# Performance work log

Measured on AMD Instinct MI355X. Metric: run time of the kernel, lower is better.

Reference implementation:

```python
import jax, jax.numpy as jnp
import numpy as np


def setup_inputs() -> dict:
    key = jax.random.key(0)
    k1, k2 = jax.random.split(key)
    x = jax.random.normal(k1, (32, 256, 32, 32), dtype=jnp.float32)
    emb = jax.random.uniform(k2, (256, 2048), dtype=jnp.float32)
    return {"x": x, "emb": emb}


def reference(x, emb):
    # x: (B, D, H, W), emb: (D, K)
    B, D = x.shape[0], x.shape[1]
    spatial = x.shape[2:]
    K = emb.shape[1]
    # flatten latents: (N, D) with N = B*H*W
    xf = jnp.moveaxis(x, 1, -1).reshape(-1, D)
    d2 = (jnp.sum(xf * xf, axis=-1, keepdims=True)
          - 2.0 * (xf @ emb)
          + jnp.sum(emb * emb, axis=0))  # (N, K)
    argmin = jnp.argmin(d2, axis=-1)  # (N,)
    q = jnp.take(emb.T, argmin, axis=0)  # (N, D) nearest codes
    out = q.reshape(B, *spatial, D)
    out = jnp.moveaxis(out, -1, 1)  # (B, D, H, W)
    return out
```

## Files before the change

### kernel.cpp

```cpp
#include <hip/hip_runtime.h>


typedef __attribute__((ext_vector_type(8))) _Float16 half8v;
typedef __attribute__((ext_vector_type(16))) float floatx16;
typedef unsigned int uint;
typedef unsigned short ushort;

#define DD 256
#define KK 2048
#define SS 1024
#define NN 32768
#define MT 64
#define NTT 256
#define LDA 24
#define MFMA_F16 __builtin_amdgcn_mfma_f32_32x32x16_f16

#define XSLAB  262144
#define XPLANE 131072
#define EPLANE 262144

union HU { _Float16 f; ushort u; };

__device__ __forceinline__ void split16(float v, ushort& h, ushort& l) {
    HU a, b;
    a.f = (_Float16)v;
    b.f = (_Float16)(v - (float)a.f);
    h = a.u; l = b.u;
}

__global__ __launch_bounds__(256) void hn_kernel(const float* __restrict__ emb,
                                                 float* __restrict__ hn) {
    int k = blockIdx.x * 256 + threadIdx.x;
    float a = 0.f;
#pragma unroll 32
    for (int d = 0; d < DD; ++d) { float e = emb[d * KK + k]; a += e * e; }
    hn[k] = 0.5f * a;
}

__global__ __launch_bounds__(256) void pack_emb(const float* __restrict__ emb,
                                                uint* __restrict__ epk) {
    int idx = blockIdx.x * 256 + threadIdx.x;
    int k = idx & (KK - 1);
    int d2 = idx >> 11;
    float a = emb[(size_t)(2 * d2) * KK + k];
    float b = emb[(size_t)(2 * d2 + 1) * KK + k];
    ushort h0, l0, h1, l1;
    split16(a, h0, l0);
    split16(b, h1, l1);
    epk[idx] = (uint)h0 | ((uint)h1 << 16);
    epk[EPLANE + idx] = (uint)l0 | ((uint)l1 << 16);
}

__global__ __launch_bounds__(256) void pack_x(const float* __restrict__ x,
                                              uint* __restrict__ px) {
    int idx = blockIdx.x * 256 + threadIdx.x;
    int s4 = idx & 255;
    int d2 = (idx >> 8) & 127;
    int bq = idx >> 15;
    const float4* xp = reinterpret_cast<const float4*>(
        x + ((size_t)(bq * DD + 2 * d2)) * SS) + s4;
    float4 a = xp[0];
    float4 b = xp[SS / 4];
    ushort h0, l0, h1, l1;
    uint4 th, tl;
    split16(a.x, h0, l0); split16(b.x, h1, l1);
    th.x = (uint)h0 | ((uint)h1 << 16); tl.x = (uint)l0 | ((uint)l1 << 16);
    split16(a.y, h0, l0); split16(b.y, h1, l1);
    th.y = (uint)h0 | ((uint)h1 << 16); tl.y = (uint)l0 | ((uint)l1 << 16);
    split16(a.z, h0, l0); split16(b.z, h1, l1);
    th.z = (uint)h0 | ((uint)h1 << 16); tl.z = (uint)l0 | ((uint)l1 << 16);
    split16(a.w, h0, l0); split16(b.w, h1, l1);
    th.w = (uint)h0 | ((uint)h1 << 16); tl.w = (uint)l0 | ((uint)l1 << 16);
    size_t o4 = (size_t)bq * (XSLAB / 4) + (size_t)d2 * (SS / 4) + s4;
    reinterpret_cast<uint4*>(px)[o4] = th;
    reinterpret_cast<uint4*>(px)[o4 + XPLANE / 4] = tl;
}

template <bool PRE>
__global__ __launch_bounds__(512, 4) void vq_fused(
        const float* __restrict__ x, const float* __restrict__ emb,
        const float* __restrict__ hn, const uint* __restrict__ epk,
        float* out) {
    __shared__ ushort Ah[2][MT * LDA], Al[2][MT * LDA];
    __shared__ ushort Bh[2][NTT * LDA], Bl[2][NTT * LDA];
    __shared__ float sv[4][MT];
    __shared__ int   sc[4][MT];
    __shared__ int   bc[MT];

    const int tid = threadIdx.x;
    const int lane = tid & 63;
    const int wid = tid >> 6;
    const int colk = lane & 31;
    const int half = lane >> 5;
    const int wm = (wid & 1) * 32;
    const int wn = (wid >> 1) * 64;

    const int base_n = blockIdx.x * MT;
    const int bq = base_n >> 10;
    const int sb = base_n & (SS - 1);

    const int lat_a = tid & 63;
    const int dqa2 = tid >> 6;
    const int cod_b = tid & 255;
    const int dqb = (tid >> 8) * 8;
    const int dqb2 = (tid >> 8) * 4;

    const float* xb = x + ((size_t)bq * DD + 2 * dqa2) * SS + sb + lat_a;
    const uint* aH = reinterpret_cast<const uint*>(out)
                     + (size_t)bq * XSLAB + (size_t)dqa2 * SS + sb + lat_a;
    const uint* eH = epk + (size_t)dqb2 * KK + cod_b;

    floatx16 acc[2];
#pragma unroll
    for (int j = 0; j < 2; ++j) acc[j] = (floatx16)(0.0f);

    float bestv[16];
    int bestc[16];
#pragma unroll
    for (int r = 0; r < 16; ++r) { bestv[r] = 3.4e38f; bestc[r] = 0; }

    float fa[2], fb[8];
    uint ua[2], ub[8];
    if constexpr (PRE) {
        ua[0] = aH[0];
        ua[1] = aH[XPLANE];
#pragma unroll
        for (int i = 0; i < 4; ++i) {
            ub[i] = eH[(size_t)i * KK];
            ub[4 + i] = eH[EPLANE + (size_t)i * KK];
        }
    } else {
        fa[0] = xb[0];
        fa[1] = xb[SS];
        const float* p = emb + (size_t)dqb * KK + cod_b;
#pragma unroll
        for (int i = 0; i < 8; ++i) fb[i] = p[(size_t)i * KK];
    }
    if constexpr (PRE) {
        *reinterpret_cast<uint*>(&Ah[0][lat_a * LDA + dqa2 * 2]) = ua[0];
        *reinterpret_cast<uint*>(&Al[0][lat_a * LDA + dqa2 * 2]) = ua[1];
        uint4 t;
        t.x = ub[0]; t.y = ub[1]; t.z = ub[2]; t.w = ub[3];
        *reinterpret_cast<uint4*>(&Bh[0][cod_b * LDA + dqb]) = t;
        t.x = ub[4]; t.y = ub[5]; t.z = ub[6]; t.w = ub[7];
        *reinterpret_cast<uint4*>(&Bl[0][cod_b * LDA + dqb]) = t;
    } else {
        ushort h[8], l[8];
        split16(fa[0], h[0], l[0]);
        split16(fa[1], h[1], l[1]);
        *reinterpret_cast<uint*>(&Ah[0][lat_a * LDA + dqa2 * 2]) =
            (uint)h[0] | ((uint)h[1] << 16);
        *reinterpret_cast<uint*>(&Al[0][lat_a * LDA + dqa2 * 2]) =
            (uint)l[0] | ((uint)l[1] << 16);
#pragma unroll
        for (int i = 0; i < 8; ++i) split16(fb[i], h[i], l[i]);
        uint4 t;
        t.x = (uint)h[0] | ((uint)h[1] << 16);
        t.y = (uint)h[2] | ((uint)h[3] << 16);
        t.z = (uint)h[4] | ((uint)h[5] << 16);
        t.w = (uint)h[6] | ((uint)h[7] << 16);
        *reinterpret_cast<uint4*>(&Bh[0][cod_b * LDA + dqb]) = t;
        t.x = (uint)l[0] | ((uint)l[1] << 16);
        t.y = (uint)l[2] | ((uint)l[3] << 16);
        t.z = (uint)l[4] | ((uint)l[5] << 16);
        t.w = (uint)l[6] | ((uint)l[7] << 16);
        *reinterpret_cast<uint4*>(&Bl[0][cod_b * LDA + dqb]) = t;
    }
    __syncthreads();

    for (int c = 0; c < 128; ++c) {
        const int cur = c & 1, nxt = cur ^ 1;
        if (c < 127) {
            const int c1 = c + 1;
            const int kt1 = c1 >> 4;
            const int dt1 = (c1 & 15) * 16;
            if constexpr (PRE) {
                const uint* pa = aH + (size_t)(dt1 >> 1) * SS;
                ua[0] = pa[0];
                ua[1] = pa[XPLANE];
                const uint* pb = eH + (size_t)(dt1 >> 1) * KK + kt1 * NTT;
#pragma unroll
                for (int i = 0; i < 4; ++i) {
                    ub[i] = pb[(size_t)i * KK];
                    ub[4 + i] = pb[EPLANE + (size_t)i * KK];
                }
            } else {
                fa[0] = xb[(size_t)dt1 * SS];
                fa[1] = xb[(size_t)dt1 * SS + SS];
                const float* p = emb + (size_t)(dt1 + dqb) * KK + kt1 * NTT + cod_b;
#pragma unroll
                for (int i = 0; i < 8; ++i) fb[i] = p[(size_t)i * KK];
            }
        }
        const int fo = colk * LDA + half * 8;
        half8v ah = *reinterpret_cast<const half8v*>(&Ah[cur][fo + wm * LDA]);
        half8v al = *reinterpret_cast<const half8v*>(&Al[cur][fo + wm * LDA]);
        half8v bh0 = *reinterpret_cast<const half8v*>(&Bh[cur][fo + wn * LDA]);
        half8v bh1 = *reinterpret_cast<const half8v*>(&Bh[cur][fo + (wn + 32) * LDA]);
        half8v bl0 = *reinterpret_cast<const half8v*>(&Bl[cur][fo + wn * LDA]);
        half8v bl1 = *reinterpret_cast<const half8v*>(&Bl[cur][fo + (wn + 32) * LDA]);

        acc[0] = MFMA_F16(ah, bh0, acc[0], 0, 0, 0);
        acc[0] = MFMA_F16(ah, bl0, acc[0], 0, 0, 0);
        acc[0] = MFMA_F16(al, bh0, acc[0], 0, 0, 0);

        acc[1] = MFMA_F16(ah, bh1, acc[1], 0, 0, 0);
        acc[1] = MFMA_F16(ah, bl1, acc[1], 0, 0, 0);
        acc[1] = MFMA_F16(al, bh1, acc[1], 0, 0, 0);

        if (c < 127) {
            if constexpr (PRE) {
                *reinterpret_cast<uint*>(&Ah[nxt][lat_a * LDA + dqa2 * 2]) = ua[0];
                *reinterpret_cast<uint*>(&Al[nxt][lat_a * LDA + dqa2 * 2]) = ua[1];
                uint4 t;
                t.x = ub[0]; t.y = ub[1]; t.z = ub[2]; t.w = ub[3];
                *reinterpret_cast<uint4*>(&Bh[nxt][cod_b * LDA + dqb]) = t;
                t.x = ub[4]; t.y = ub[5]; t.z = ub[6]; t.w = ub[7];
                *reinterpret_cast<uint4*>(&Bl[nxt][cod_b * LDA + dqb]) = t;
            } else {
                ushort h[8], l[8];
                split16(fa[0], h[0], l[0]);
                split16(fa[1], h[1], l[1]);
                *reinterpret_cast<uint*>(&Ah[nxt][lat_a * LDA + dqa2 * 2]) =
                    (uint)h[0] | ((uint)h[1] << 16);
                *reinterpret_cast<uint*>(&Al[nxt][lat_a * LDA + dqa2 * 2]) =
                    (uint)l[0] | ((uint)l[1] << 16);
#pragma unroll
                for (int i = 0; i < 8; ++i) split16(fb[i], h[i], l[i]);
                uint4 t;
                t.x = (uint)h[0] | ((uint)h[1] << 16);
                t.y = (uint)h[2] | ((uint)h[3] << 16);
                t.z = (uint)h[4] | ((uint)h[5] << 16);
                t.w = (uint)h[6] | ((uint)h[7] << 16);
                *reinterpret_cast<uint4*>(&Bh[nxt][cod_b * LDA + dqb]) = t;
                t.x = (uint)l[0] | ((uint)l[1] << 16);
                t.y = (uint)l[2] | ((uint)l[3] << 16);
                t.z = (uint)l[4] | ((uint)l[5] << 16);
                t.w = (uint)l[6] | ((uint)l[7] << 16);
                *reinterpret_cast<uint4*>(&Bl[nxt][cod_b * LDA + dqb]) = t;
            }
        }
        if ((c & 15) == 15) {
            const int kt = c >> 4;
            const int cd0 = kt * NTT + wn + colk;
            const int cd1 = cd0 + 32;
            const float h0 = hn[cd0];
            const float h1 = hn[cd1];
#pragma unroll
            for (int r = 0; r < 16; ++r) {
                float s0 = h0 - acc[0][r];
                float s1 = h1 - acc[1][r];
                float v = s0; int cd = cd0;
                if (s1 < s0) { v = s1; cd = cd1; }
                if (v < bestv[r]) { bestv[r] = v; bestc[r] = cd; }
                acc[0][r] = 0.f;
                acc[1][r] = 0.f;
            }
        }
        __syncthreads();
    }

#pragma unroll
    for (int r = 0; r < 16; ++r) {
        float v = bestv[r];
        int cd = bestc[r];
#pragma unroll
        for (int mk = 1; mk < 32; mk <<= 1) {
            float ov = __shfl_xor(v, mk);
            int oc = __shfl_xor(cd, mk);
            if (ov < v || (ov == v && oc < cd)) { v = ov; cd = oc; }
        }
        if (colk == 0) {
            const int row = (r & 3) + 8 * (r >> 2) + 4 * half;
            sv[wid >> 1][wm + row] = v;
            sc[wid >> 1][wm + row] = cd;
        }
    }
    __syncthreads();
    if (tid < MT) {
        float v = sv[0][tid]; int cd = sc[0][tid];
#pragma unroll
        for (int g = 1; g < 4; ++g) {
            float ov = sv[g][tid]; int oc = sc[g][tid];
            if (ov < v || (ov == v && oc < cd)) { v = ov; cd = oc; }
        }
        bc[tid] = cd;
    }
    __syncthreads();
    {
        const int mq = tid & 15;
        const int dg = tid >> 4;
        const int k0 = bc[mq * 4 + 0];
        const int k1 = bc[mq * 4 + 1];
        const int k2 = bc[mq * 4 + 2];
        const int k3 = bc[mq * 4 + 3];
#pragma unroll 4
        for (int dd = 0; dd < 8; ++dd) {
            const int d = dg * 8 + dd;
            const float* er = emb + (size_t)d * KK;
            float4 o = make_float4(er[k0], er[k1], er[k2], er[k3]);
            reinterpret_cast<float4*>(&out[((size_t)bq * DD + d) * SS + sb])[mq] = o;
        }
    }
}

extern "C" void kernel_launch(void* const* d_in, const int* in_sizes, int n_in,
                              void* d_out, int out_size, void* d_ws, size_t ws_size,
                              hipStream_t stream) {
    const float* x = (const float*)d_in[0];
    const float* emb = (const float*)d_in[1];
    float* out = (float*)d_out;
    float* hn = (float*)d_ws;
    uint* epk = (uint*)((char*)d_ws + KK * sizeof(float));

    const size_t need = (size_t)KK * 4 + (size_t)2 * EPLANE * 4;

    hipLaunchKernelGGL(hn_kernel, dim3(KK / 256), dim3(256), 0, stream, emb, hn);
    if (ws_size >= need) {
        hipLaunchKernelGGL(pack_emb, dim3(EPLANE / 256), dim3(256), 0, stream,
                           emb, epk);
        hipLaunchKernelGGL(pack_x, dim3(4096), dim3(256), 0, stream,
                           x, (uint*)out);
        hipLaunchKernelGGL((vq_fused<true>), dim3(NN / MT), dim3(512), 0, stream,
                           x, emb, hn, epk, out);
    } else {
        hipLaunchKernelGGL((vq_fused<false>), dim3(NN / MT), dim3(512), 0, stream,
                           x, emb, hn, epk, out);
    }
}
```

Measured before the change: 262.3 us.

## Load MFMA fragments directly from global memory, dropping LDS staging and pack_x

Replaces the LDS double-buffered GEMM with a kernel where each lane loads its MFMA A and B fragments straight from global memory into registers, prefetching one step ahead. x is split into fp16 hi/lo in registers, so the separate pack_x pass and its round trip through the output buffer go away. Per-iteration __syncthreads and LDS traffic are removed. The cost is redundant global loads across waves (A is reread by the 4 N-waves, B by the 2 M-waves), which now rely on L1/L2 hits, plus more register pressure from the prefetch buffers.

```diff
diff --git a/kernel.cpp b/kernel.cpp
--- a/kernel.cpp
+++ b/kernel.cpp
@@ -20,6 +20,7 @@
 #define EPLANE 262144
 
 union HU { _Float16 f; ushort u; };
+union FragU { uint u[4]; half8v v; };
 
 __device__ __forceinline__ void split16(float v, ushort& h, ushort& l) {
     HU a, b;
@@ -51,38 +52,10 @@
     epk[EPLANE + idx] = (uint)l0 | ((uint)l1 << 16);
 }
 
-__global__ __launch_bounds__(256) void pack_x(const float* __restrict__ x,
-                                              uint* __restrict__ px) {
-    int idx = blockIdx.x * 256 + threadIdx.x;
-    int s4 = idx & 255;
-    int d2 = (idx >> 8) & 127;
-    int bq = idx >> 15;
-    const float4* xp = reinterpret_cast<const float4*>(
-        x + ((size_t)(bq * DD + 2 * d2)) * SS) + s4;
-    float4 a = xp[0];
-    float4 b = xp[SS / 4];
-    ushort h0, l0, h1, l1;
-    uint4 th, tl;
-    split16(a.x, h0, l0); split16(b.x, h1, l1);
-    th.x = (uint)h0 | ((uint)h1 << 16); tl.x = (uint)l0 | ((uint)l1 << 16);
-    split16(a.y, h0, l0); split16(b.y, h1, l1);
-    th.y = (uint)h0 | ((uint)h1 << 16); tl.y = (uint)l0 | ((uint)l1 << 16);
-    split16(a.z, h0, l0); split16(b.z, h1, l1);
-    th.z = (uint)h0 | ((uint)h1 << 16); tl.z = (uint)l0 | ((uint)l1 << 16);
-    split16(a.w, h0, l0); split16(b.w, h1, l1);
-    th.w = (uint)h0 | ((uint)h1 << 16); tl.w = (uint)l0 | ((uint)l1 << 16);
-    size_t o4 = (size_t)bq * (XSLAB / 4) + (size_t)d2 * (SS / 4) + s4;
-    reinterpret_cast<uint4*>(px)[o4] = th;
-    reinterpret_cast<uint4*>(px)[o4 + XPLANE / 4] = tl;
-}
-
-template <bool PRE>
-__global__ __launch_bounds__(512, 4) void vq_fused(
-        const float* __restrict__ x, const float* __restrict__ emb,
-        const float* __restrict__ hn, const uint* __restrict__ epk,
-        float* out) {
-    __shared__ ushort Ah[2][MT * LDA], Al[2][MT * LDA];
-    __shared__ ushort Bh[2][NTT * LDA], Bl[2][NTT * LDA];
+__global__ __launch_bounds__(512, 4) void vq_direct(
+        const float* __restrict__ x, const uint* __restrict__ epk,
+        const float* __restrict__ hn, const float* __restrict__ emb,
+        float* __restrict__ out) {
     __shared__ float sv[4][MT];
     __shared__ int   sc[4][MT];
     __shared__ int   bc[MT];
@@ -92,23 +65,16 @@
     const int wid = tid >> 6;
     const int colk = lane & 31;
     const int half = lane >> 5;
-    const int wm = (wid & 1) * 32;
-    const int wn = (wid >> 1) * 64;
+    const int wm = __builtin_amdgcn_readfirstlane((wid & 1) * 32);
+    const int wn = __builtin_amdgcn_readfirstlane((wid >> 1) * 64);
 
     const int base_n = blockIdx.x * MT;
     const int bq = base_n >> 10;
     const int sb = base_n & (SS - 1);
 
-    const int lat_a = tid & 63;
-    const int dqa2 = tid >> 6;
-    const int cod_b = tid & 255;
-    const int dqb = (tid >> 8) * 8;
-    const int dqb2 = (tid >> 8) * 4;
-
-    const float* xb = x + ((size_t)bq * DD + 2 * dqa2) * SS + sb + lat_a;
-    const uint* aH = reinterpret_cast<const uint*>(out)
-                     + (size_t)bq * XSLAB + (size_t)dqa2 * SS + sb + lat_a;
-    const uint* eH = epk + (size_t)dqb2 * KK + cod_b;
+    const float* xA = x + ((size_t)bq * DD + half * 8) * SS + (sb + wm + colk);
+    const int oB0 = half * 4 * KK + wn + colk;
+    const int oB1 = oB0 + 32;
 
     floatx16 acc[2];
 #pragma unroll
@@ -119,127 +85,62 @@
 #pragma unroll
     for (int r = 0; r < 16; ++r) { bestv[r] = 3.4e38f; bestc[r] = 0; }
 
-    float fa[2], fb[8];
-    uint ua[2], ub[8];
-    if constexpr (PRE) {
-        ua[0] = aH[0];
-        ua[1] = aH[XPLANE];
-#pragma unroll
-        for (int i = 0; i < 4; ++i) {
-            ub[i] = eH[(size_t)i * KK];
-            ub[4 + i] = eH[EPLANE + (size_t)i * KK];
-        }
-    } else {
-        fa[0] = xb[0];
-        fa[1] = xb[SS];
-        const float* p = emb + (size_t)dqb * KK + cod_b;
-#pragma unroll
-        for (int i = 0; i < 8; ++i) fb[i] = p[(size_t)i * KK];
-    }
-    if constexpr (PRE) {
-        *reinterpret_cast<uint*>(&Ah[0][lat_a * LDA + dqa2 * 2]) = ua[0];
-        *reinterpret_cast<uint*>(&Al[0][lat_a * LDA + dqa2 * 2]) = ua[1];
-        uint4 t;
-        t.x = ub[0]; t.y = ub[1]; t.z = ub[2]; t.w = ub[3];
-        *reinterpret_cast<uint4*>(&Bh[0][cod_b * LDA + dqb]) = t;
-        t.x = ub[4]; t.y = ub[5]; t.z = ub[6]; t.w = ub[7];
-        *reinterpret_cast<uint4*>(&Bl[0][cod_b * LDA + dqb]) = t;
-    } else {
-        ushort h[8], l[8];
-        split16(fa[0], h[0], l[0]);
-        split16(fa[1], h[1], l[1]);
-        *reinterpret_cast<uint*>(&Ah[0][lat_a * LDA + dqa2 * 2]) =
-            (uint)h[0] | ((uint)h[1] << 16);
-        *reinterpret_cast<uint*>(&Al[0][lat_a * LDA + dqa2 * 2]) =
-            (uint)l[0] | ((uint)l[1] << 16);
-#pragma unroll
-        for (int i = 0; i < 8; ++i) split16(fb[i], h[i], l[i]);
-        uint4 t;
-        t.x = (uint)h[0] | ((uint)h[1] << 16);
-        t.y = (uint)h[2] | ((uint)h[3] << 16);
-        t.z = (uint)h[4] | ((uint)h[5] << 16);
-        t.w = (uint)h[6] | ((uint)h[7] << 16);
-        *reinterpret_cast<uint4*>(&Bh[0][cod_b * LDA + dqb]) = t;
-        t.x = (uint)l[0] | ((uint)l[1] << 16);
-        t.y = (uint)l[2] | ((uint)l[3] << 16);
-        t.z = (uint)l[4] | ((uint)l[5] << 16);
-        t.w = (uint)l[6] | ((uint)l[7] << 16);
-        *reinterpret_cast<uint4*>(&Bl[0][cod_b * LDA + dqb]) = t;
-    }
-    __syncthreads();
-
+    float fa[8], pa[8];
+    uint rbh[2][4], rbl[2][4];
+    uint pbh[2][4], pbl[2][4];
+
+#pragma unroll
+    for (int j = 0; j < 8; ++j) fa[j] = xA[(size_t)j * SS];
+    {
+        const uint* uB = epk;
+#pragma unroll
+        for (int j = 0; j < 4; ++j) {
+            rbh[0][j] = uB[oB0 + (size_t)j * KK];
+            rbh[1][j] = uB[oB1 + (size_t)j * KK];
+            rbl[0][j] = uB[(size_t)EPLANE + oB0 + (size_t)j * KK];
+            rbl[1][j] = uB[(size_t)EPLANE + oB1 + (size_t)j * KK];
+        }
+    }
+
+#pragma unroll 2
     for (int c = 0; c < 128; ++c) {
-        const int cur = c & 1, nxt = cur ^ 1;
         if (c < 127) {
             const int c1 = c + 1;
             const int kt1 = c1 >> 4;
-            const int dt1 = (c1 & 15) * 16;
-            if constexpr (PRE) {
-                const uint* pa = aH + (size_t)(dt1 >> 1) * SS;
-                ua[0] = pa[0];
-                ua[1] = pa[XPLANE];
-                const uint* pb = eH + (size_t)(dt1 >> 1) * KK + kt1 * NTT;
-#pragma unroll
-                for (int i = 0; i < 4; ++i) {
-                    ub[i] = pb[(size_t)i * KK];
-                    ub[4 + i] = pb[EPLANE + (size_t)i * KK];
-                }
-            } else {
-                fa[0] = xb[(size_t)dt1 * SS];
-                fa[1] = xb[(size_t)dt1 * SS + SS];
-                const float* p = emb + (size_t)(dt1 + dqb) * KK + kt1 * NTT + cod_b;
-#pragma unroll
-                for (int i = 0; i < 8; ++i) fb[i] = p[(size_t)i * KK];
+            const int dh1 = (c1 & 15) * 8;
+            const float* pxa = xA + (size_t)(dh1 * 2) * SS;
+#pragma unroll
+            for (int j = 0; j < 8; ++j) pa[j] = pxa[(size_t)j * SS];
+            const uint* uB = epk + (size_t)dh1 * KK + kt1 * NTT;
+#pragma unroll
+            for (int j = 0; j < 4; ++j) {
+                pbh[0][j] = uB[oB0 + (size_t)j * KK];
+                pbh[1][j] = uB[oB1 + (size_t)j * KK];
+                pbl[0][j] = uB[(size_t)EPLANE + oB0 + (size_t)j * KK];
+                pbl[1][j] = uB[(size_t)EPLANE + oB1 + (size_t)j * KK];
             }
         }
-        const int fo = colk * LDA + half * 8;
-        half8v ah = *reinterpret_cast<const half8v*>(&Ah[cur][fo + wm * LDA]);
-        half8v al = *reinterpret_cast<const half8v*>(&Al[cur][fo + wm * LDA]);
-        half8v bh0 = *reinterpret_cast<const half8v*>(&Bh[cur][fo + wn * LDA]);
-        half8v bh1 = *reinterpret_cast<const half8v*>(&Bh[cur][fo + (wn + 32) * LDA]);
-        half8v bl0 = *reinterpret_cast<const half8v*>(&Bl[cur][fo + wn * LDA]);
-        half8v bl1 = *reinterpret_cast<const half8v*>(&Bl[cur][fo + (wn + 32) * LDA]);
-
-        acc[0] = MFMA_F16(ah, bh0, acc[0], 0, 0, 0);
-        acc[0] = MFMA_F16(ah, bl0, acc[0], 0, 0, 0);
-        acc[0] = MFMA_F16(al, bh0, acc[0], 0, 0, 0);
-
-        acc[1] = MFMA_F16(ah, bh1, acc[1], 0, 0, 0);
-        acc[1] = MFMA_F16(ah, bl1, acc[1], 0, 0, 0);
-        acc[1] = MFMA_F16(al, bh1, acc[1], 0, 0, 0);
-
-        if (c < 127) {
-            if constexpr (PRE) {
-                *reinterpret_cast<uint*>(&Ah[nxt][lat_a * LDA + dqa2 * 2]) = ua[0];
-                *reinterpret_cast<uint*>(&Al[nxt][lat_a * LDA + dqa2 * 2]) = ua[1];
-                uint4 t;
-                t.x = ub[0]; t.y = ub[1]; t.z = ub[2]; t.w = ub[3];
-                *reinterpret_cast<uint4*>(&Bh[nxt][cod_b * LDA + dqb]) = t;
-                t.x = ub[4]; t.y = ub[5]; t.z = ub[6]; t.w = ub[7];
-                *reinterpret_cast<uint4*>(&Bl[nxt][cod_b * LDA + dqb]) = t;
-            } else {
-                ushort h[8], l[8];
-                split16(fa[0], h[0], l[0]);
-                split16(fa[1], h[1], l[1]);
-                *reinterpret_cast<uint*>(&Ah[nxt][lat_a * LDA + dqa2 * 2]) =
-                    (uint)h[0] | ((uint)h[1] << 16);
-                *reinterpret_cast<uint*>(&Al[nxt][lat_a * LDA + dqa2 * 2]) =
-                    (uint)l[0] | ((uint)l[1] << 16);
-#pragma unroll
-                for (int i = 0; i < 8; ++i) split16(fb[i], h[i], l[i]);
-                uint4 t;
-                t.x = (uint)h[0] | ((uint)h[1] << 16);
-                t.y = (uint)h[2] | ((uint)h[3] << 16);
-                t.z = (uint)h[4] | ((uint)h[5] << 16);
-                t.w = (uint)h[6] | ((uint)h[7] << 16);
-                *reinterpret_cast<uint4*>(&Bh[nxt][cod_b * LDA + dqb]) = t;
-                t.x = (uint)l[0] | ((uint)l[1] << 16);
-                t.y = (uint)l[2] | ((uint)l[3] << 16);
-                t.z = (uint)l[4] | ((uint)l[5] << 16);
-                t.w = (uint)l[6] | ((uint)l[7] << 16);
-                *reinterpret_cast<uint4*>(&Bl[nxt][cod_b * LDA + dqb]) = t;
-            }
-        }
+        ushort h[8], l[8];
+#pragma unroll
+        for (int j = 0; j < 8; ++j) split16(fa[j], h[j], l[j]);
+        FragU ah, al, b0h, b1h, b0l, b1l;
+#pragma unroll
+        for (int j = 0; j < 4; ++j) {
+            ah.u[j] = (uint)h[2 * j] | ((uint)h[2 * j + 1] << 16);
+            al.u[j] = (uint)l[2 * j] | ((uint)l[2 * j + 1] << 16);
+            b0h.u[j] = rbh[0][j];
+            b1h.u[j] = rbh[1][j];
+            b0l.u[j] = rbl[0][j];
+            b1l.u[j] = rbl[1][j];
+        }
+        acc[0] = MFMA_F16(ah.v, b0h.v, acc[0], 0, 0, 0);
+        acc[0] = MFMA_F16(ah.v, b0l.v, acc[0], 0, 0, 0);
+        acc[0] = MFMA_F16(al.v, b0h.v, acc[0], 0, 0, 0);
+
+        acc[1] = MFMA_F16(ah.v, b1h.v, acc[1], 0, 0, 0);
+        acc[1] = MFMA_F16(ah.v, b1l.v, acc[1], 0, 0, 0);
+        acc[1] = MFMA_F16(al.v, b1h.v, acc[1], 0, 0, 0);
+
         if ((c & 15) == 15) {
             const int kt = c >> 4;
             const int cd0 = kt * NTT + wn + colk;
@@ -257,7 +158,17 @@
                 acc[1][r] = 0.f;
             }
         }
-        __syncthreads();
+        if (c < 127) {
+#pragma unroll
+            for (int j = 0; j < 8; ++j) fa[j] = pa[j];
+#pragma unroll
+            for (int j = 0; j < 4; ++j) {
+                rbh[0][j] = pbh[0][j];
+                rbh[1][j] = pbh[1][j];
+                rbl[0][j] = pbl[0][j];
+                rbl[1][j] = pbl[1][j];
+            }
+        }
     }
 
 #pragma unroll
@@ -304,6 +215,191 @@
     }
 }
 
+template <bool PRE>
+__global__ __launch_bounds__(512, 4) void vq_fused(
+        const float* __restrict__ x, const float* __restrict__ emb,
+        const float* __restrict__ hn, const uint* __restrict__ epk,
+        float* out) {
+    __shared__ ushort Ah[2][MT * LDA], Al[2][MT * LDA];
+    __shared__ ushort Bh[2][NTT * LDA], Bl[2][NTT * LDA];
+    __shared__ float sv[4][MT];
+    __shared__ int   sc[4][MT];
+    __shared__ int   bc[MT];
+
+    const int tid = threadIdx.x;
+    const int lane = tid & 63;
+    const int wid = tid >> 6;
+    const int colk = lane & 31;
+    const int half = lane >> 5;
+    const int wm = (wid & 1) * 32;
+    const int wn = (wid >> 1) * 64;
+
+    const int base_n = blockIdx.x * MT;
+    const int bq = base_n >> 10;
+    const int sb = base_n & (SS - 1);
+
+    const int lat_a = tid & 63;
+    const int dqa2 = tid >> 6;
+    const int cod_b = tid & 255;
+    const int dqb = (tid >> 8) * 8;
+
+    const float* xb = x + ((size_t)bq * DD + 2 * dqa2) * SS + sb + lat_a;
+
+    floatx16 acc[2];
+#pragma unroll
+    for (int j = 0; j < 2; ++j) acc[j] = (floatx16)(0.0f);
+
+    float bestv[16];
+    int bestc[16];
+#pragma unroll
+    for (int r = 0; r < 16; ++r) { bestv[r] = 3.4e38f; bestc[r] = 0; }
+
+    float fa[2], fb[8];
+    fa[0] = xb[0];
+    fa[1] = xb[SS];
+    {
+        const float* p = emb + (size_t)dqb * KK + cod_b;
+#pragma unroll
+        for (int i = 0; i < 8; ++i) fb[i] = p[(size_t)i * KK];
+    }
+    {
+        ushort h[8], l[8];
+        split16(fa[0], h[0], l[0]);
+        split16(fa[1], h[1], l[1]);
+        *reinterpret_cast<uint*>(&Ah[0][lat_a * LDA + dqa2 * 2]) =
+            (uint)h[0] | ((uint)h[1] << 16);
+        *reinterpret_cast<uint*>(&Al[0][lat_a * LDA + dqa2 * 2]) =
+            (uint)l[0] | ((uint)l[1] << 16);
+#pragma unroll
+        for (int i = 0; i < 8; ++i) split16(fb[i], h[i], l[i]);
+        uint4 t;
+        t.x = (uint)h[0] | ((uint)h[1] << 16);
+        t.y = (uint)h[2] | ((uint)h[3] << 16);
+        t.z = (uint)h[4] | ((uint)h[5] << 16);
+        t.w = (uint)h[6] | ((uint)h[7] << 16);
+        *reinterpret_cast<uint4*>(&Bh[0][cod_b * LDA + dqb]) = t;
+        t.x = (uint)l[0] | ((uint)l[1] << 16);
+        t.y = (uint)l[2] | ((uint)l[3] << 16);
+        t.z = (uint)l[4] | ((uint)l[5] << 16);
+        t.w = (uint)l[6] | ((uint)l[7] << 16);
+        *reinterpret_cast<uint4*>(&Bl[0][cod_b * LDA + dqb]) = t;
+    }
+    __syncthreads();
+
+    for (int c = 0; c < 128; ++c) {
+        const int cur = c & 1, nxt = cur ^ 1;
+        if (c < 127) {
+            const int c1 = c + 1;
+            const int kt1 = c1 >> 4;
+            const int dt1 = (c1 & 15) * 16;
+            fa[0] = xb[(size_t)dt1 * SS];
+            fa[1] = xb[(size_t)dt1 * SS + SS];
+            const float* p = emb + (size_t)(dt1 + dqb) * KK + kt1 * NTT + cod_b;
+#pragma unroll
+            for (int i = 0; i < 8; ++i) fb[i] = p[(size_t)i * KK];
+        }
+        const int fo = colk * LDA + half * 8;
+        half8v ah = *reinterpret_cast<const half8v*>(&Ah[cur][fo + wm * LDA]);
+        half8v al = *reinterpret_cast<const half8v*>(&Al[cur][fo + wm * LDA]);
+        half8v bh0 = *reinterpret_cast<const half8v*>(&Bh[cur][fo + wn * LDA]);
+        half8v bh1 = *reinterpret_cast<const half8v*>(&Bh[cur][fo + (wn + 32) * LDA]);
+        half8v bl0 = *reinterpret_cast<const half8v*>(&Bl[cur][fo + wn * LDA]);
+        half8v bl1 = *reinterpret_cast<const half8v*>(&Bl[cur][fo + (wn + 32) * LDA]);
+
+        acc[0] = MFMA_F16(ah, bh0, acc[0], 0, 0, 0);
+        acc[0] = MFMA_F16(ah, bl0, acc[0], 0, 0, 0);
+        acc[0] = MFMA_F16(al, bh0, acc[0], 0, 0, 0);
+
+        acc[1] = MFMA_F16(ah, bh1, acc[1], 0, 0, 0);
+        acc[1] = MFMA_F16(ah, bl1, acc[1], 0, 0, 0);
+        acc[1] = MFMA_F16(al, bh1, acc[1], 0, 0, 0);
+
+        if (c < 127) {
+            ushort h[8], l[8];
+            split16(fa[0], h[0], l[0]);
+            split16(fa[1], h[1], l[1]);
+            *reinterpret_cast<uint*>(&Ah[nxt][lat_a * LDA + dqa2 * 2]) =
+                (uint)h[0] | ((uint)h[1] << 16);
+            *reinterpret_cast<uint*>(&Al[nxt][lat_a * LDA + dqa2 * 2]) =
+                (uint)l[0] | ((uint)l[1] << 16);
+#pragma unroll
+            for (int i = 0; i < 8; ++i) split16(fb[i], h[i], l[i]);
+            uint4 t;
+            t.x = (uint)h[0] | ((uint)h[1] << 16);
+            t.y = (uint)h[2] | ((uint)h[3] << 16);
+            t.z = (uint)h[4] | ((uint)h[5] << 16);
+            t.w = (uint)h[6] | ((uint)h[7] << 16);
+            *reinterpret_cast<uint4*>(&Bh[nxt][cod_b * LDA + dqb]) = t;
+            t.x = (uint)l[0] | ((uint)l[1] << 16);
+            t.y = (uint)l[2] | ((uint)l[3] << 16);
+            t.z = (uint)l[4] | ((uint)l[5] << 16);
+            t.w = (uint)l[6] | ((uint)l[7] << 16);
+            *reinterpret_cast<uint4*>(&Bl[nxt][cod_b * LDA + dqb]) = t;
+        }
+        if ((c & 15) == 15) {
+            const int kt = c >> 4;
+            const int cd0 = kt * NTT + wn + colk;
+            const int cd1 = cd0 + 32;
+            const float h0 = hn[cd0];
+            const float h1 = hn[cd1];
+#pragma unroll
+            for (int r = 0; r < 16; ++r) {
+                float s0 = h0 - acc[0][r];
+                float s1 = h1 - acc[1][r];
+                float v = s0; int cd = cd0;
+                if (s1 < s0) { v = s1; cd = cd1; }
+                if (v < bestv[r]) { bestv[r] = v; bestc[r] = cd; }
+                acc[0][r] = 0.f;
+                acc[1][r] = 0.f;
+            }
+        }
+        __syncthreads();
+    }
+
+#pragma unroll
+    for (int r = 0; r < 16; ++r) {
+        float v = bestv[r];
+        int cd = bestc[r];
+#pragma unroll
+        for (int mk = 1; mk < 32; mk <<= 1) {
+            float ov = __shfl_xor(v, mk);
+            int oc = __shfl_xor(cd, mk);
+            if (ov < v || (ov == v && oc < cd)) { v = ov; cd = oc; }
+        }
+        if (colk == 0) {
+            const int row = (r & 3) + 8 * (r >> 2) + 4 * half;
+            sv[wid >> 1][wm + row] = v;
+            sc[wid >> 1][wm + row] = cd;
+        }
+    }
+    __syncthreads();
+    if (tid < MT) {
+        float v = sv[0][tid]; int cd = sc[0][tid];
+#pragma unroll
+        for (int g = 1; g < 4; ++g) {
+            float ov = sv[g][tid]; int oc = sc[g][tid];
+            if (ov < v || (ov == v && oc < cd)) { v = ov; cd = oc; }
+        }
+        bc[tid] = cd;
+    }
+    __syncthreads();
+    {
+        const int mq = tid & 15;
+        const int dg = tid >> 4;
+        const int k0 = bc[mq * 4 + 0];
+        const int k1 = bc[mq * 4 + 1];
+        const int k2 = bc[mq * 4 + 2];
+        const int k3 = bc[mq * 4 + 3];
+#pragma unroll 4
+        for (int dd = 0; dd < 8; ++dd) {
+            const int d = dg * 8 + dd;
+            const float* er = emb + (size_t)d * KK;
+            float4 o = make_float4(er[k0], er[k1], er[k2], er[k3]);
+            reinterpret_cast<float4*>(&out[((size_t)bq * DD + d) * SS + sb])[mq] = o;
+        }
+    }
+}
+
 extern "C" void kernel_launch(void* const* d_in, const int* in_sizes, int n_in,
                               void* d_out, int out_size, void* d_ws, size_t ws_size,
                               hipStream_t stream) {
@@ -319,10 +415,8 @@
     if (ws_size >= need) {
         hipLaunchKernelGGL(pack_emb, dim3(EPLANE / 256), dim3(256), 0, stream,
                            emb, epk);
-        hipLaunchKernelGGL(pack_x, dim3(4096), dim3(256), 0, stream,
-                           x, (uint*)out);
-        hipLaunchKernelGGL((vq_fused<true>), dim3(NN / MT), dim3(512), 0, stream,
-                           x, emb, hn, epk, out);
+        hipLaunchKernelGGL(vq_direct, dim3(NN / MT), dim3(512), 0, stream,
+                           x, epk, hn, emb, out);
     } else {
         hipLaunchKernelGGL((vq_fused<false>), dim3(NN / MT), dim3(512), 0, stream,
                            x, emb, hn, epk, out);
```

Result: slower. 295.1 us (+12.5%).

## Double latent tile to 128 with 1024-thread blocks, drop x prepack, parallelize hn

Applied to the files above, without the earlier changes.

The fused VQ kernel now handles 128 latents per block with 16 waves. Each staged codebook tile is reused across twice as many rows, so codebook global loads per latent are halved. The separate pack_x pass and its round trip through the output buffer are removed; x is loaded and split into fp16 hi/lo parts inside the main loop. The hn kernel now splits the D reduction across 8 thread groups and combines them in shared memory. Risks are 1024-thread blocks with launch_bounds min 4 (register pressure, possible spills), lower occupancy and half as many blocks.

```diff
diff --git a/kernel.cpp b/kernel.cpp
--- a/kernel.cpp
+++ b/kernel.cpp
@@ -10,13 +10,11 @@
 #define KK 2048
 #define SS 1024
 #define NN 32768
-#define MT 64
+#define MT 128
 #define NTT 256
 #define LDA 24
 #define MFMA_F16 __builtin_amdgcn_mfma_f32_32x32x16_f16
 
-#define XSLAB  262144
-#define XPLANE 131072
 #define EPLANE 262144
 
 union HU { _Float16 f; ushort u; };
@@ -30,11 +28,24 @@
 
 __global__ __launch_bounds__(256) void hn_kernel(const float* __restrict__ emb,
                                                  float* __restrict__ hn) {
-    int k = blockIdx.x * 256 + threadIdx.x;
+    __shared__ float red[256];
+    const int tid = threadIdx.x;
+    const int k = blockIdx.x * 32 + (tid & 31);
+    const int j = tid >> 5;
     float a = 0.f;
-#pragma unroll 32
-    for (int d = 0; d < DD; ++d) { float e = emb[d * KK + k]; a += e * e; }
-    hn[k] = 0.5f * a;
+#pragma unroll
+    for (int i = 0; i < 32; ++i) {
+        float e = emb[(size_t)(j * 32 + i) * KK + k];
+        a += e * e;
+    }
+    red[tid] = a;
+    __syncthreads();
+    if (j == 0) {
+        float s = a;
+#pragma unroll
+        for (int g = 1; g < 8; ++g) s += red[g * 32 + (tid & 31)];
+        hn[k] = 0.5f * s;
+    }
 }
 
 __global__ __launch_bounds__(256) void pack_emb(const float* __restrict__ emb,
@@ -51,36 +62,11 @@
     epk[EPLANE + idx] = (uint)l0 | ((uint)l1 << 16);
 }
 
-__global__ __launch_bounds__(256) void pack_x(const float* __restrict__ x,
-                                              uint* __restrict__ px) {
-    int idx = blockIdx.x * 256 + threadIdx.x;
-    int s4 = idx & 255;
-    int d2 = (idx >> 8) & 127;
-    int bq = idx >> 15;
-    const float4* xp = reinterpret_cast<const float4*>(
-        x + ((size_t)(bq * DD + 2 * d2)) * SS) + s4;
-    float4 a = xp[0];
-    float4 b = xp[SS / 4];
-    ushort h0, l0, h1, l1;
-    uint4 th, tl;
-    split16(a.x, h0, l0); split16(b.x, h1, l1);
-    th.x = (uint)h0 | ((uint)h1 << 16); tl.x = (uint)l0 | ((uint)l1 << 16);
-    split16(a.y, h0, l0); split16(b.y, h1, l1);
-    th.y = (uint)h0 | ((uint)h1 << 16); tl.y = (uint)l0 | ((uint)l1 << 16);
-    split16(a.z, h0, l0); split16(b.z, h1, l1);
-    th.z = (uint)h0 | ((uint)h1 << 16); tl.z = (uint)l0 | ((uint)l1 << 16);
-    split16(a.w, h0, l0); split16(b.w, h1, l1);
-    th.w = (uint)h0 | ((uint)h1 << 16); tl.w = (uint)l0 | ((uint)l1 << 16);
-    size_t o4 = (size_t)bq * (XSLAB / 4) + (size_t)d2 * (SS / 4) + s4;
-    reinterpret_cast<uint4*>(px)[o4] = th;
-    reinterpret_cast<uint4*>(px)[o4 + XPLANE / 4] = tl;
-}
-
 template <bool PRE>
-__global__ __launch_bounds__(512, 4) void vq_fused(
+__global__ __launch_bounds__(1024, 4) void vq_fused(
         const float* __restrict__ x, const float* __restrict__ emb,
         const float* __restrict__ hn, const uint* __restrict__ epk,
-        float* out) {
+        float* __restrict__ out) {
     __shared__ ushort Ah[2][MT * LDA], Al[2][MT * LDA];
     __shared__ ushort Bh[2][NTT * LDA], Bl[2][NTT * LDA];
     __shared__ float sv[4][MT];
@@ -92,23 +78,19 @@
     const int wid = tid >> 6;
     const int colk = lane & 31;
     const int half = lane >> 5;
-    const int wm = (wid & 1) * 32;
-    const int wn = (wid >> 1) * 64;
+    const int wm = (wid & 3) * 32;
+    const int wn = (wid >> 2) * 64;
 
     const int base_n = blockIdx.x * MT;
     const int bq = base_n >> 10;
     const int sb = base_n & (SS - 1);
 
-    const int lat_a = tid & 63;
-    const int dqa2 = tid >> 6;
+    const int lat_a = tid & 127;
+    const int d2a = tid >> 7;
     const int cod_b = tid & 255;
-    const int dqb = (tid >> 8) * 8;
-    const int dqb2 = (tid >> 8) * 4;
-
-    const float* xb = x + ((size_t)bq * DD + 2 * dqa2) * SS + sb + lat_a;
-    const uint* aH = reinterpret_cast<const uint*>(out)
-                     + (size_t)bq * XSLAB + (size_t)dqa2 * SS + sb + lat_a;
-    const uint* eH = epk + (size_t)dqb2 * KK + cod_b;
+    const int qb = tid >> 8;
+
+    const float* xA = x + ((size_t)bq * DD + 2 * d2a) * SS + sb + lat_a;
 
     floatx16 acc[2];
 #pragma unroll
@@ -119,52 +101,46 @@
 #pragma unroll
     for (int r = 0; r < 16; ++r) { bestv[r] = 3.4e38f; bestc[r] = 0; }
 
-    float fa[2], fb[8];
-    uint ua[2], ub[8];
+    float fa[2];
+    uint ub[4];
+    float fb[4];
+
+    fa[0] = xA[0];
+    fa[1] = xA[SS];
     if constexpr (PRE) {
-        ua[0] = aH[0];
-        ua[1] = aH[XPLANE];
-#pragma unroll
-        for (int i = 0; i < 4; ++i) {
-            ub[i] = eH[(size_t)i * KK];
-            ub[4 + i] = eH[EPLANE + (size_t)i * KK];
-        }
+        const uint* uB = epk + (size_t)(2 * qb) * KK + cod_b;
+        ub[0] = uB[0];
+        ub[1] = uB[KK];
+        ub[2] = uB[EPLANE];
+        ub[3] = uB[EPLANE + KK];
     } else {
-        fa[0] = xb[0];
-        fa[1] = xb[SS];
-        const float* p = emb + (size_t)dqb * KK + cod_b;
-#pragma unroll
-        for (int i = 0; i < 8; ++i) fb[i] = p[(size_t)i * KK];
-    }
-    if constexpr (PRE) {
-        *reinterpret_cast<uint*>(&Ah[0][lat_a * LDA + dqa2 * 2]) = ua[0];
-        *reinterpret_cast<uint*>(&Al[0][lat_a * LDA + dqa2 * 2]) = ua[1];
-        uint4 t;
-        t.x = ub[0]; t.y = ub[1]; t.z = ub[2]; t.w = ub[3];
-        *reinterpret_cast<uint4*>(&Bh[0][cod_b * LDA + dqb]) = t;
-        t.x = ub[4]; t.y = ub[5]; t.z = ub[6]; t.w = ub[7];
-        *reinterpret_cast<uint4*>(&Bl[0][cod_b * LDA + dqb]) = t;
-    } else {
-        ushort h[8], l[8];
-        split16(fa[0], h[0], l[0]);
-        split16(fa[1], h[1], l[1]);
-        *reinterpret_cast<uint*>(&Ah[0][lat_a * LDA + dqa2 * 2]) =
-            (uint)h[0] | ((uint)h[1] << 16);
-        *reinterpret_cast<uint*>(&Al[0][lat_a * LDA + dqa2 * 2]) =
-            (uint)l[0] | ((uint)l[1] << 16);
-#pragma unroll
-        for (int i = 0; i < 8; ++i) split16(fb[i], h[i], l[i]);
-        uint4 t;
-        t.x = (uint)h[0] | ((uint)h[1] << 16);
-        t.y = (uint)h[2] | ((uint)h[3] << 16);
-        t.z = (uint)h[4] | ((uint)h[5] << 16);
-        t.w = (uint)h[6] | ((uint)h[7] << 16);
-        *reinterpret_cast<uint4*>(&Bh[0][cod_b * LDA + dqb]) = t;
-        t.x = (uint)l[0] | ((uint)l[1] << 16);
-        t.y = (uint)l[2] | ((uint)l[3] << 16);
-        t.z = (uint)l[4] | ((uint)l[5] << 16);
-        t.w = (uint)l[6] | ((uint)l[7] << 16);
-        *reinterpret_cast<uint4*>(&Bl[0][cod_b * LDA + dqb]) = t;
+        const float* p = emb + (size_t)(4 * qb) * KK + cod_b;
+#pragma unroll
+        for (int i = 0; i < 4; ++i) fb[i] = p[(size_t)i * KK];
+    }
+    {
+        ushort h0, l0, h1, l1;
+        split16(fa[0], h0, l0);
+        split16(fa[1], h1, l1);
+        *reinterpret_cast<uint*>(&Ah[0][lat_a * LDA + 2 * d2a]) =
+            (uint)h0 | ((uint)h1 << 16);
+        *reinterpret_cast<uint*>(&Al[0][lat_a * LDA + 2 * d2a]) =
+            (uint)l0 | ((uint)l1 << 16);
+        uint2 wh, wl;
+        if constexpr (PRE) {
+            wh.x = ub[0]; wh.y = ub[1];
+            wl.x = ub[2]; wl.y = ub[3];
+        } else {
+            ushort h[4], l[4];
+#pragma unroll
+            for (int i = 0; i < 4; ++i) split16(fb[i], h[i], l[i]);
+            wh.x = (uint)h[0] | ((uint)h[1] << 16);
+            wh.y = (uint)h[2] | ((uint)h[3] << 16);
+            wl.x = (uint)l[0] | ((uint)l[1] << 16);
+            wl.y = (uint)l[2] | ((uint)l[3] << 16);
+        }
+        *reinterpret_cast<uint2*>(&Bh[0][cod_b * LDA + 4 * qb]) = wh;
+        *reinterpret_cast<uint2*>(&Bl[0][cod_b * LDA + 4 * qb]) = wl;
     }
     __syncthreads();
 
@@ -174,22 +150,20 @@
             const int c1 = c + 1;
             const int kt1 = c1 >> 4;
             const int dt1 = (c1 & 15) * 16;
+            fa[0] = xA[(size_t)dt1 * SS];
+            fa[1] = xA[(size_t)dt1 * SS + SS];
             if constexpr (PRE) {
-                const uint* pa = aH + (size_t)(dt1 >> 1) * SS;
-                ua[0] = pa[0];
-                ua[1] = pa[XPLANE];
-                const uint* pb = eH + (size_t)(dt1 >> 1) * KK + kt1 * NTT;
-#pragma unroll
-                for (int i = 0; i < 4; ++i) {
-                    ub[i] = pb[(size_t)i * KK];
-                    ub[4 + i] = pb[EPLANE + (size_t)i * KK];
-                }
+                const uint* uB = epk + (size_t)(dt1 / 2 + 2 * qb) * KK
+                                 + kt1 * NTT + cod_b;
+                ub[0] = uB[0];
+                ub[1] = uB[KK];
+                ub[2] = uB[EPLANE];
+                ub[3] = uB[EPLANE + KK];
             } else {
-                fa[0] = xb[(size_t)dt1 * SS];
-                fa[1] = xb[(size_t)dt1 * SS + SS];
-                const float* p = emb + (size_t)(dt1 + dqb) * KK + kt1 * NTT + cod_b;
-#pragma unroll
-                for (int i = 0; i < 8; ++i) fb[i] = p[(size_t)i * KK];
+                const float* p = emb + (size_t)(dt1 + 4 * qb) * KK
+                                 + kt1 * NTT + cod_b;
+#pragma unroll
+                for (int i = 0; i < 4; ++i) fb[i] = p[(size_t)i * KK];
             }
         }
         const int fo = colk * LDA + half * 8;
@@ -209,36 +183,28 @@
         acc[1] = MFMA_F16(al, bh1, acc[1], 0, 0, 0);
 
         if (c < 127) {
+            ushort h0, l0, h1, l1;
+            split16(fa[0], h0, l0);
+            split16(fa[1], h1, l1);
+            *reinterpret_cast<uint*>(&Ah[nxt][lat_a * LDA + 2 * d2a]) =
+                (uint)h0 | ((uint)h1 << 16);
+            *reinterpret_cast<uint*>(&Al[nxt][lat_a * LDA + 2 * d2a]) =
+                (uint)l0 | ((uint)l1 << 16);
+            uint2 wh, wl;
             if constexpr (PRE) {
-                *reinterpret_cast<uint*>(&Ah[nxt][lat_a * LDA + dqa2 * 2]) = ua[0];
-                *reinterpret_cast<uint*>(&Al[nxt][lat_a * LDA + dqa2 * 2]) = ua[1];
-                uint4 t;
-                t.x = ub[0]; t.y = ub[1]; t.z = ub[2]; t.w = ub[3];
-                *reinterpret_cast<uint4*>(&Bh[nxt][cod_b * LDA + dqb]) = t;
-                t.x = ub[4]; t.y = ub[5]; t.z = ub[6]; t.w = ub[7];
-                *reinterpret_cast<uint4*>(&Bl[nxt][cod_b * LDA + dqb]) = t;
+                wh.x = ub[0]; wh.y = ub[1];
+                wl.x = ub[2]; wl.y = ub[3];
             } else {
-                ushort h[8], l[8];
-                split16(fa[0], h[0], l[0]);
-                split16(fa[1], h[1], l[1]);
-                *reinterpret_cast<uint*>(&Ah[nxt][lat_a * LDA + dqa2 * 2]) =
-                    (uint)h[0] | ((uint)h[1] << 16);
-                *reinterpret_cast<uint*>(&Al[nxt][lat_a * LDA + dqa2 * 2]) =
-                    (uint)l[0] | ((uint)l[1] << 16);
-#pragma unroll
-                for (int i = 0; i < 8; ++i) split16(fb[i], h[i], l[i]);
-                uint4 t;
-                t.x = (uint)h[0] | ((uint)h[1] << 16);
-                t.y = (uint)h[2] | ((uint)h[3] << 16);
-                t.z = (uint)h[4] | ((uint)h[5] << 16);
-                t.w = (uint)h[6] | ((uint)h[7] << 16);
-                *reinterpret_cast<uint4*>(&Bh[nxt][cod_b * LDA + dqb]) = t;
-                t.x = (uint)l[0] | ((uint)l[1] << 16);
-                t.y = (uint)l[2] | ((uint)l[3] << 16);
-                t.z = (uint)l[4] | ((uint)l[5] << 16);
-                t.w = (uint)l[6] | ((uint)l[7] << 16);
-                *reinterpret_cast<uint4*>(&Bl[nxt][cod_b * LDA + dqb]) = t;
+                ushort h[4], l[4];
+#pragma unroll
+                for (int i = 0; i < 4; ++i) split16(fb[i], h[i], l[i]);
+                wh.x = (uint)h[0] | ((uint)h[1] << 16);
+                wh.y = (uint)h[2] | ((uint)h[3] << 16);
+                wl.x = (uint)l[0] | ((uint)l[1] << 16);
+                wl.y = (uint)l[2] | ((uint)l[3] << 16);
             }
+            *reinterpret_cast<uint2*>(&Bh[nxt][cod_b * LDA + 4 * qb]) = wh;
+            *reinterpret_cast<uint2*>(&Bl[nxt][cod_b * LDA + 4 * qb]) = wl;
         }
         if ((c & 15) == 15) {
             const int kt = c >> 4;
@@ -272,8 +238,8 @@
         }
         if (colk == 0) {
             const int row = (r & 3) + 8 * (r >> 2) + 4 * half;
-            sv[wid >> 1][wm + row] = v;
-            sc[wid >> 1][wm + row] = cd;
+            sv[wid >> 2][wm + row] = v;
+            sc[wid >> 2][wm + row] = cd;
         }
     }
     __syncthreads();
@@ -288,8 +254,8 @@
     }
     __syncthreads();
     {
-        const int mq = tid & 15;
-        const int dg = tid >> 4;
+        const int mq = tid & 31;
+        const int dg = tid >> 5;
         const int k0 = bc[mq * 4 + 0];
         const int k1 = bc[mq * 4 + 1];
         const int k2 = bc[mq * 4 + 2];
@@ -315,16 +281,14 @@
 
     const size_t need = (size_t)KK * 4 + (size_t)2 * EPLANE * 4;
 
-    hipLaunchKernelGGL(hn_kernel, dim3(KK / 256), dim3(256), 0, stream, emb, hn);
+    hipLaunchKernelGGL(hn_kernel, dim3(KK / 32), dim3(256), 0, stream, emb, hn);
     if (ws_size >= need) {
         hipLaunchKernelGGL(pack_emb, dim3(EPLANE / 256), dim3(256), 0, stream,
                            emb, epk);
-        hipLaunchKernelGGL(pack_x, dim3(4096), dim3(256), 0, stream,
-                           x, (uint*)out);
-        hipLaunchKernelGGL((vq_fused<true>), dim3(NN / MT), dim3(512), 0, stream,
+        hipLaunchKernelGGL((vq_fused<true>), dim3(NN / MT), dim3(1024), 0, stream,
                            x, emb, hn, epk, out);
     } else {
-        hipLaunchKernelGGL((vq_fused<false>), dim3(NN / MT), dim3(512), 0, stream,
+        hipLaunchKernelGGL((vq_fused<false>), dim3(NN / MT), dim3(1024), 0, stream,
                            x, emb, hn, epk, out);
     }
 }
```

After: 235.9 us. -10.1%, faster.
